# Kernel optimization log

Measured on AMD Instinct MI355X. Metric: run time of the kernel, lower is better.

## Reference

```python
import jax, jax.numpy as jnp
import numpy as np

N = 50000      # nodes
E = 800000     # edges (before self-loops)
F_IN = 512     # input features
H = 8          # heads (layer 1)
C = 32         # hidden per head
CLS = 40       # classes


def setup_inputs() -> dict:
    key = jax.random.key(0)
    ks = jax.random.split(key, 10)
    small = lambda k, shape: jax.random.normal(k, shape, jnp.float32) * 0.05
    return {
        "x": jax.random.normal(ks[0], (N, F_IN), jnp.float32),
        "edge_index": jax.random.randint(ks[1], (2, E), 0, N, jnp.int32),
        # layer 1 params (GATConv: F_IN -> C per head, 8 heads, concat)
        "W1": small(ks[2], (F_IN, H * C)),
        "a_src1": small(ks[3], (H, C)),
        "a_dst1": small(ks[4], (H, C)),
        "b1": jnp.zeros((H * C,), jnp.float32),
        # layer 2 params (GATConv: H*C -> CLS, 1 head)
        "W2": small(ks[5], (H * C, CLS)),
        "a_src2": small(ks[6], (1, CLS)),
        "a_dst2": small(ks[7], (1, CLS)),
        "b2": jnp.zeros((CLS,), jnp.float32),
    }


def gat_conv(x, W, a_src, a_dst, b, src, dst, n):
    """PyG-style GATConv (negative_slope=0.2); self-loops already in src/dst."""
    h_, c_ = a_src.shape
    h = (x @ W).reshape(n, h_, c_)                       # [N, H, C]
    alpha_src = jnp.einsum('nhc,hc->nh', h, a_src)       # [N, H]
    alpha_dst = jnp.einsum('nhc,hc->nh', h, a_dst)       # [N, H]
    e = jax.nn.leaky_relu(alpha_src[src] + alpha_dst[dst], 0.2)  # [E', H]
    # segment softmax over incoming edges of each destination node
    m = jax.lax.stop_gradient(jax.ops.segment_max(e, dst, num_segments=n))
    ex = jnp.exp(e - m[dst])
    den = jax.ops.segment_sum(ex, dst, num_segments=n)
    alpha = ex / (den[dst] + 1e-16)                      # [E', H]
    out = jax.ops.segment_sum(h[src] * alpha[:, :, None], dst, num_segments=n)
    return out.reshape(n, h_ * c_) + b


def reference(x, edge_index, W1, a_src1, a_dst1, b1, W2, a_src2, a_dst2, b2):
    n = x.shape[0]
    loop = jnp.arange(n, dtype=edge_index.dtype)
    src = jnp.concatenate([edge_index[0], loop])  # add self-loops (PyG default)
    dst = jnp.concatenate([edge_index[1], loop])
    # dropout is identity at inference
    h = jax.nn.elu(gat_conv(x, W1, a_src1, a_dst1, b1, src, dst, n))
    out = gat_conv(h, W2, a_src2, a_dst2, b2, src, dst, n)
    return jax.nn.log_softmax(out, axis=1)
```

## Files before the change

kernel.cpp:

```cpp
#include <hip/hip_runtime.h>
#include <hip/hip_bf16.h>
#include <math.h>

constexpr int NN  = 50000;
constexpr int NE  = 800000;
constexpr int EP  = NE + NN;
constexpr int FIN = 512;
constexpr int NH  = 8;
constexpr int NC  = 32;
constexpr int HC  = NH * NC;
constexpr int CLS = 40;
constexpr int CLSP = 48;
constexpr int NGB = (NN + 63) / 64;
constexpr int NSCB = (EP + 255) / 256;
constexpr int CVTW_ITEMS = HC * (FIN / 8) + CLSP * HC;
constexpr int CVTW_B = (CVTW_ITEMS + 255) / 256;

typedef __attribute__((ext_vector_type(8))) __bf16 bf16x8;
typedef __attribute__((ext_vector_type(4))) __bf16 bf16x4;
typedef __attribute__((ext_vector_type(4))) float f32x4;
typedef __attribute__((ext_vector_type(2))) float f32x2;

__device__ inline bf16x8 cvt8v(const f32x4 a, const f32x4 b) {
  bf16x8 o;
  o[0] = (__bf16)a.x; o[1] = (__bf16)a.y; o[2] = (__bf16)a.z; o[3] = (__bf16)a.w;
  o[4] = (__bf16)b.x; o[5] = (__bf16)b.y; o[6] = (__bf16)b.z; o[7] = (__bf16)b.w;
  return o;
}

__device__ inline unsigned char to_fp8(float f) {
  int pk = __builtin_amdgcn_cvt_pk_fp8_f32(f, f, 0, false);
  return (unsigned char)(pk & 0xff);
}

__device__ inline float from_fp8(unsigned char b) {
  f32x2 v = __builtin_amdgcn_cvt_pk_f32_fp8((unsigned)b, false);
  return v.x;
}

__global__ void k_prep(const int* __restrict__ ei, int* __restrict__ deg,
                       const float* __restrict__ W1, const float* __restrict__ W2,
                       __bf16* __restrict__ Wt, __bf16* __restrict__ W2t) {
  if (blockIdx.x < NSCB) {
    int e = blockIdx.x * 256 + threadIdx.x;
    if (e >= EP) return;
    int d = (e < NE) ? ei[NE + e] : (e - NE);
    atomicAdd(&deg[d], 1);
    return;
  }
  int t = (blockIdx.x - NSCB) * 256 + threadIdx.x;
  if (t < HC * (FIN / 8)) {
    int c = t >> 6, kq = (t & 63) * 8;
    bf16x8 o;
#pragma unroll
    for (int j = 0; j < 8; ++j) o[j] = (__bf16)W1[(size_t)(kq + j) * HC + c];
    *(bf16x8*)&Wt[(size_t)c * FIN + kq] = o;
  } else if (t < CVTW_ITEMS) {
    int u = t - HC * (FIN / 8);
    int c = u >> 8, k = u & 255;
    W2t[u] = (c < CLS) ? (__bf16)W2[(size_t)k * CLS + c] : (__bf16)0.f;
  }
}

__global__ __launch_bounds__(1024) void k_scan1(const int* __restrict__ deg,
                                                int* __restrict__ rowptr1,
                                                int* __restrict__ bsum, int n) {
  __shared__ int sm[1024];
  int i = blockIdx.x * 1024 + threadIdx.x;
  int v = (i < n) ? deg[i] : 0;
  sm[threadIdx.x] = v;
  __syncthreads();
  for (int off = 1; off < 1024; off <<= 1) {
    int t = (threadIdx.x >= off) ? sm[threadIdx.x - off] : 0;
    __syncthreads();
    sm[threadIdx.x] += t;
    __syncthreads();
  }
  if (i < n) rowptr1[i] = sm[threadIdx.x];
  if (threadIdx.x == 1023) bsum[blockIdx.x] = sm[1023];
}

__global__ void k_scan2(int* __restrict__ bsum, int nb) {
  int lane = threadIdx.x;
  int v = (lane < nb) ? bsum[lane] : 0;
#pragma unroll
  for (int off = 1; off < 64; off <<= 1) {
    int t = __shfl_up(v, off);
    if (lane >= off) v += t;
  }
  int ex = __shfl_up(v, 1);
  if (lane == 0) ex = 0;
  if (lane < nb) bsum[lane] = ex;
}

__global__ void k_scan3(int* __restrict__ rowptr, const int* __restrict__ bsum,
                        int* __restrict__ cursor, int n) {
  int i = blockIdx.x * 256 + threadIdx.x;
  if (i == 0) { rowptr[0] = 0; cursor[0] = 0; }
  if (i < n) {
    int v = rowptr[i + 1] + bsum[i >> 10];
    rowptr[i + 1] = v;
    if (i + 1 < n) cursor[i + 1] = v;
  }
}

__global__ __launch_bounds__(256) void k_gemm1_scatter(
    const float* __restrict__ X, const __bf16* __restrict__ Wt,
    const float* __restrict__ a_s1, const float* __restrict__ a_d1,
    unsigned char* __restrict__ Hout, float* __restrict__ asrc1,
    float* __restrict__ adst1,
    const int* __restrict__ ei, int* __restrict__ cursor,
    unsigned short* __restrict__ srcS) {
  __shared__ __align__(16) float Xp[2][4096];
  const int tid = threadIdx.x;

  if (blockIdx.x >= NGB) {
    int e = (blockIdx.x - NGB) * 256 + tid;
    if (e < EP) {
      int s, d;
      if (e < NE) { s = ei[e]; d = ei[NE + e]; } else { s = d = e - NE; }
      int p = atomicAdd(&cursor[d], 1);
      srcS[p] = (unsigned short)s;
    }
    return;
  }

  const int lane = tid & 63;
  const int w    = tid >> 6;
  const int wn   = w * 64;
  const int bm   = blockIdx.x * 64;
  const int l15  = lane & 15, lg = lane >> 4;

  const int srow_l  = (lane >> 4);
  const int sslot   = (l15 >> 1);
  const int shalf   = (lane & 1);

  f32x4 acc[4][4] = {};

  auto issue = [&](int c, int buf) {
#pragma unroll
    for (int jj = 0; jj < 4; ++jj) {
      const int j = w * 4 + jj;
      const int row_l = 4 * j + srow_l;
      const int rowG = min(bm + row_l, NN - 1);
      const int g = sslot ^ (row_l & 7);
      const float* src = X + (size_t)rowG * FIN + c * 64 + g * 8 + shalf * 4;
      __builtin_amdgcn_global_load_lds(
          (const __attribute__((address_space(1))) void*)src,
          (__attribute__((address_space(3))) void*)(&Xp[buf][j * 256]), 16, 0, 0);
    }
  };

  issue(0, 0);
  for (int c = 0; c < 8; ++c) {
    const int cur = c & 1;
    __syncthreads();
    if (c < 7) issue(c + 1, cur ^ 1);

#pragma unroll
    for (int kh = 0; kh < 2; ++kh) {
      const int kb = lg + 4 * kh;
      bf16x8 bv[4];
#pragma unroll
      for (int ni = 0; ni < 4; ++ni)
        bv[ni] = *(const bf16x8*)(Wt + (size_t)(wn + ni * 16 + l15) * FIN
                                     + c * 64 + kb * 8);
#pragma unroll
      for (int mi = 0; mi < 4; ++mi) {
        int r = mi * 16 + l15;
        int fo = r * 64 + ((kb ^ (r & 7)) << 3);
        f32x4 alo = *(const f32x4*)&Xp[cur][fo];
        f32x4 ahi = *(const f32x4*)&Xp[cur][fo + 4];
        bf16x8 av = cvt8v(alo, ahi);
#pragma unroll
        for (int ni = 0; ni < 4; ++ni)
          acc[mi][ni] = __builtin_amdgcn_mfma_f32_16x16x32_bf16(
              av, bv[ni], acc[mi][ni], 0, 0, 0);
      }
    }
    __syncthreads();
  }

  const int hbase = 2 * w;
#pragma unroll
  for (int hh = 0; hh < 2; ++hh) {
    float asA = a_s1[(hbase + hh) * NC + l15];
    float asB = a_s1[(hbase + hh) * NC + 16 + l15];
    float adA = a_d1[(hbase + hh) * NC + l15];
    float adB = a_d1[(hbase + hh) * NC + 16 + l15];
    float vs = 0.f, vd = 0.f;
#pragma unroll
    for (int mi = 0; mi < 4; ++mi) {
#pragma unroll
      for (int r = 0; r < 4; ++r) {
        float ps = acc[mi][2 * hh][r] * asA + acc[mi][2 * hh + 1][r] * asB;
        float pd = acc[mi][2 * hh][r] * adA + acc[mi][2 * hh + 1][r] * adB;
#pragma unroll
        for (int off = 1; off < 16; off <<= 1) {
          ps += __shfl_xor(ps, off, 64);
          pd += __shfl_xor(pd, off, 64);
        }
        if (l15 == mi * 4 + r) { vs = ps; vd = pd; }
      }
    }
    int rw = bm + (l15 >> 2) * 16 + lg * 4 + (l15 & 3);
    if (rw < NN) {
      asrc1[(size_t)rw * NH + hbase + hh] = vs;
      adst1[(size_t)rw * NH + hbase + hh] = vd;
    }
  }

#pragma unroll
  for (int mi = 0; mi < 4; ++mi) {
#pragma unroll
    for (int ni = 0; ni < 4; ++ni) {
      int col = wn + ni * 16 + l15;
#pragma unroll
      for (int r = 0; r < 4; ++r) {
        int row = bm + mi * 16 + lg * 4 + r;
        if (row < NN) Hout[(size_t)row * HC + col] = to_fp8(acc[mi][ni][r]);
      }
    }
  }
}

__global__ __launch_bounds__(256) void k_agg1(const unsigned char* __restrict__ h1f8,
                                              const float* __restrict__ asrc,
                                              const float* __restrict__ adst,
                                              const unsigned short* __restrict__ srcS,
                                              const int* __restrict__ rowptr,
                                              const float* __restrict__ b1,
                                              __bf16* __restrict__ helu) {
  int wave = (blockIdx.x * 256 + threadIdx.x) >> 6;
  int lane = threadIdx.x & 63;
  if (wave >= NN) return;
  int lo = rowptr[wave], hi = rowptr[wave + 1];
  int head = lane >> 3;
  int hw   = lane & 7;
  float adstv = adst[wave * NH + head];
  float ad2   = adst[wave * NH + hw];
  float4 acc = {0.f, 0.f, 0.f, 0.f};
  float den = 0.f;

  for (int base = lo; base < hi; base += 64) {
    int cnt = hi - base; if (cnt > 64) cnt = 64;
    int sv = (lane < cnt) ? (int)srcS[base + lane] : 0;
    int j = 0;
    for (; j + 8 <= cnt; j += 8) {
      int se = __shfl(sv, j + head);
      float v = asrc[se * NH + hw] + ad2;
      v = v > 0.f ? v : 0.2f * v;
      float wv = __expf(v);
      int s[8]; unsigned int hv[8];
#pragma unroll
      for (int u = 0; u < 8; ++u) s[u] = __shfl(sv, j + u);
#pragma unroll
      for (int u = 0; u < 8; ++u)
        hv[u] = *(const unsigned int*)&h1f8[(size_t)s[u] * HC + lane * 4];
#pragma unroll
      for (int u = 0; u < 8; ++u) {
        float wu = __shfl(wv, u * 8 + head);
        f32x2 lo2 = __builtin_amdgcn_cvt_pk_f32_fp8(hv[u], false);
        f32x2 hi2 = __builtin_amdgcn_cvt_pk_f32_fp8(hv[u], true);
        acc.x += wu * lo2.x;
        acc.y += wu * lo2.y;
        acc.z += wu * hi2.x;
        acc.w += wu * hi2.y;
        den += wu;
      }
    }
    for (; j < cnt; ++j) {
      int s = __shfl(sv, j);
      float v = asrc[s * NH + head] + adstv;
      v = v > 0.f ? v : 0.2f * v;
      float w = __expf(v);
      unsigned int hv = *(const unsigned int*)&h1f8[(size_t)s * HC + lane * 4];
      f32x2 lo2 = __builtin_amdgcn_cvt_pk_f32_fp8(hv, false);
      f32x2 hi2 = __builtin_amdgcn_cvt_pk_f32_fp8(hv, true);
      acc.x += w * lo2.x;
      acc.y += w * lo2.y;
      acc.z += w * hi2.x;
      acc.w += w * hi2.y;
      den += w;
    }
  }

  float inv = 1.f / (den + 1e-16f);
  float4 bb = *(const float4*)&b1[lane * 4];
  float o[4] = {acc.x * inv + bb.x, acc.y * inv + bb.y,
                acc.z * inv + bb.z, acc.w * inv + bb.w};
  bf16x4 ov;
#pragma unroll
  for (int j2 = 0; j2 < 4; ++j2) {
    float e = o[j2] > 0.f ? o[j2] : expm1f(o[j2]);
    ov[j2] = (__bf16)e;
  }
  *(bf16x4*)&helu[(size_t)wave * HC + lane * 4] = ov;
}

__global__ __launch_bounds__(256) void k_gemm2m(const __bf16* __restrict__ A,
                                                const __bf16* __restrict__ W2t,
                                                const float* __restrict__ a_s2,
                                                const float* __restrict__ a_d2,
                                                unsigned char* __restrict__ h2p,
                                                float* __restrict__ asrc2,
                                                float* __restrict__ adst2) {
  __shared__ __align__(16) __bf16 As[128 * 8 * 8];
  __shared__ __align__(16) __bf16 Bsh[CLSP * 33 * 8];
  const int tid  = threadIdx.x;
  const int lane = tid & 63;
  const int w    = tid >> 6;
  const int wm   = w * 32;
  const int bm   = blockIdx.x * 128;

  const int l3 = lane >> 3;
  const int l7 = lane & 7;
  const int kb_src = l7 ^ l3;

  for (int s = tid; s < CLSP * 32; s += 256) {
    int c = s >> 5, kb = s & 31;
    *(bf16x8*)(Bsh + (size_t)(c * 33 + kb) * 8) =
        *(const bf16x8*)(W2t + (size_t)c * HC + kb * 8);
  }

  f32x4 acc[2][3] = {};

  for (int step = 0; step < 4; ++step) {
    const int k0 = step * 64;
#pragma unroll
    for (int q = 0; q < 4; ++q) {
      const int inst = w * 4 + q;
      const int r = inst * 8 + l3;
      const int arow = min(bm + r, NN - 1);
      const __bf16* ga = A + (size_t)arow * HC + k0 + kb_src * 8;
      __builtin_amdgcn_global_load_lds(
          (const __attribute__((address_space(1))) void*)ga,
          (__attribute__((address_space(3))) void*)(As + inst * 512), 16, 0, 0);
    }
    __syncthreads();

    const int l15 = lane & 15, lg = lane >> 4;
#pragma unroll
    for (int kh = 0; kh < 2; ++kh) {
      const int kbl = lg + 4 * kh;
      const int kbg = step * 8 + kbl;
      bf16x8 av[2], bv[3];
#pragma unroll
      for (int mi = 0; mi < 2; ++mi) {
        int r = wm + mi * 16 + l15;
        av[mi] = *(const bf16x8*)(As + (size_t)(r * 8 + (kbl ^ (r & 7))) * 8);
      }
#pragma unroll
      for (int ni = 0; ni < 3; ++ni) {
        int c = ni * 16 + l15;
        bv[ni] = *(const bf16x8*)(Bsh + (size_t)(c * 33 + kbg) * 8);
      }
#pragma unroll
      for (int mi = 0; mi < 2; ++mi)
#pragma unroll
        for (int ni = 0; ni < 3; ++ni)
          acc[mi][ni] = __builtin_amdgcn_mfma_f32_16x16x32_bf16(
              av[mi], bv[ni], acc[mi][ni], 0, 0, 0);
    }
    __syncthreads();
  }

  const int l15 = lane & 15, lg = lane >> 4;

  {
    int c0 = l15, c1 = 16 + l15, c2 = 32 + l15;
    float as0 = a_s2[c0], as1 = a_s2[c1], as2v = (c2 < CLS) ? a_s2[c2] : 0.f;
    float ad0 = a_d2[c0], ad1 = a_d2[c1], ad2v = (c2 < CLS) ? a_d2[c2] : 0.f;
    float vs = 0.f, vd = 0.f;
#pragma unroll
    for (int mi = 0; mi < 2; ++mi) {
#pragma unroll
      for (int r = 0; r < 4; ++r) {
        float ps = acc[mi][0][r] * as0 + acc[mi][1][r] * as1 + acc[mi][2][r] * as2v;
        float pd = acc[mi][0][r] * ad0 + acc[mi][1][r] * ad1 + acc[mi][2][r] * ad2v;
#pragma unroll
        for (int off = 1; off < 16; off <<= 1) {
          ps += __shfl_xor(ps, off, 64);
          pd += __shfl_xor(pd, off, 64);
        }
        if (l15 == mi * 4 + r) { vs = ps; vd = pd; }
      }
    }
    int rw = bm + wm + (l15 >> 2) * 16 + lg * 4 + (l15 & 3);
    if (l15 < 8 && rw < NN) {
      asrc2[rw] = vs;
      adst2[rw] = vd;
    }
  }

#pragma unroll
  for (int mi = 0; mi < 2; ++mi) {
#pragma unroll
    for (int ni = 0; ni < 3; ++ni) {
      int col = ni * 16 + l15;
      if (col >= CLS) continue;
#pragma unroll
      for (int r = 0; r < 4; ++r) {
        int row = bm + wm + mi * 16 + lg * 4 + r;
        if (row < NN) h2p[(size_t)row * 64 + col] = to_fp8(acc[mi][ni][r]);
      }
    }
  }
}

__global__ __launch_bounds__(256) void k_agg2(const unsigned char* __restrict__ h2p,
                                              const float* __restrict__ asrc,
                                              const float* __restrict__ adst,
                                              const unsigned short* __restrict__ srcS,
                                              const int* __restrict__ rowptr,
                                              const float* __restrict__ b2,
                                              float* __restrict__ out) {
  int wave = (blockIdx.x * 256 + threadIdx.x) >> 6;
  int lane = threadIdx.x & 63;
  if (wave >= NN) return;
  int lo = rowptr[wave], hi = rowptr[wave + 1];
  bool act = lane < CLS;
  float adstv = adst[wave];
  float acc = 0.f, den = 0.f;

  for (int base = lo; base < hi; base += 64) {
    int cnt = hi - base; if (cnt > 64) cnt = 64;
    int sv = (lane < cnt) ? (int)srcS[base + lane] : 0;
    float v = asrc[sv] + adstv;
    v = v > 0.f ? v : 0.2f * v;
    float wv = __expf(v);
    int j = 0;
    for (; j + 8 <= cnt; j += 8) {
      int s[8]; float hval[8];
#pragma unroll
      for (int u = 0; u < 8; ++u) s[u] = __shfl(sv, j + u);
#pragma unroll
      for (int u = 0; u < 8; ++u)
        hval[u] = act ? from_fp8(h2p[(size_t)s[u] * 64 + lane]) : 0.f;
#pragma unroll
      for (int u = 0; u < 8; ++u) {
        float wu = __shfl(wv, j + u);
        acc += wu * hval[u];
        den += wu;
      }
    }
    for (; j < cnt; ++j) {
      int s = __shfl(sv, j);
      float wu = __shfl(wv, j);
      if (act) acc += wu * from_fp8(h2p[(size_t)s * 64 + lane]);
      den += wu;
    }
  }

  float o = act ? (acc / (den + 1e-16f) + b2[lane]) : -INFINITY;
  float m = o;
#pragma unroll
  for (int off = 32; off; off >>= 1) m = fmaxf(m, __shfl_xor(m, off, 64));
  float ex = act ? __expf(o - m) : 0.f;
  float ssum = ex;
#pragma unroll
  for (int off = 32; off; off >>= 1) ssum += __shfl_xor(ssum, off, 64);
  if (act) out[(size_t)wave * CLS + lane] = o - m - logf(ssum);
}

extern "C" void kernel_launch(void* const* d_in, const int* in_sizes, int n_in,
                              void* d_out, int out_size, void* d_ws, size_t ws_size,
                              hipStream_t stream) {
  const float* x      = (const float*)d_in[0];
  const int*   ei     = (const int*)d_in[1];
  const float* W1     = (const float*)d_in[2];
  const float* a_src1 = (const float*)d_in[3];
  const float* a_dst1 = (const float*)d_in[4];
  const float* b1     = (const float*)d_in[5];
  const float* W2     = (const float*)d_in[6];
  const float* a_src2 = (const float*)d_in[7];
  const float* a_dst2 = (const float*)d_in[8];
  const float* b2     = (const float*)d_in[9];
  float* out = (float*)d_out;

  char* p = (char*)d_ws;
  auto alloc = [&](size_t bytes) {
    char* r = p;
    p += (bytes + 255) & ~size_t(255);
    return r;
  };
  unsigned char* h1f8 = (unsigned char*)alloc((size_t)NN * HC);
  __bf16* helu  = (__bf16*)alloc((size_t)NN * HC * 2);
  __bf16* Wt    = (__bf16*)alloc((size_t)HC * FIN * 2);
  __bf16* W2t   = (__bf16*)alloc((size_t)CLSP * HC * 2);
  unsigned char* h2p = (unsigned char*)alloc((size_t)NN * 64);
  float*  asrc1 = (float*)alloc((size_t)NN * NH * 4);
  float*  adst1 = (float*)alloc((size_t)NN * NH * 4);
  float*  asrc2 = (float*)alloc((size_t)NN * 4);
  float*  adst2 = (float*)alloc((size_t)NN * 4);
  unsigned short* srcS = (unsigned short*)alloc((size_t)EP * 2);
  int*    deg   = (int*)alloc((size_t)NN * 4);
  int*    cursor= (int*)alloc((size_t)NN * 4);
  int*    rowptr= (int*)alloc((size_t)(NN + 1) * 4);
  int*    bsum  = (int*)alloc(256 * 4);

  hipMemsetAsync(deg, 0, (size_t)NN * 4, stream);

  const int nbScan = (NN + 1023) / 1024;
  k_prep<<<NSCB + CVTW_B, 256, 0, stream>>>(ei, deg, W1, W2, Wt, W2t);
  k_scan1<<<nbScan, 1024, 0, stream>>>(deg, rowptr + 1, bsum, NN);
  k_scan2<<<1, 64, 0, stream>>>(bsum, nbScan);
  k_scan3<<<(NN + 255) / 256, 256, 0, stream>>>(rowptr, bsum, cursor, NN);

  k_gemm1_scatter<<<NGB + NSCB, 256, 0, stream>>>(x, Wt, a_src1, a_dst1,
                                                  h1f8, asrc1, adst1,
                                                  ei, cursor, srcS);

  k_agg1<<<(NN + 3) / 4, 256, 0, stream>>>(h1f8, asrc1, adst1, srcS, rowptr, b1, helu);

  k_gemm2m<<<(NN + 127) / 128, 256, 0, stream>>>(helu, W2t, a_src2, a_dst2,
                                                 h2p, asrc2, adst2);

  k_agg2<<<(NN + 3) / 4, 256, 0, stream>>>(h2p, asrc2, adst2, srcS, rowptr, b2, out);
}
```

Before: 226.3 us.

## Restructure CSR build: histogram with per-edge rank overlapped with GEMM1, then atomic-free scatter

The degree histogram moves into the GEMM1 kernel and records each edge's atomic rank. After the scan, a separate pass places sources at rowptr[d]+rank[e] with no atomics. This removes the second atomic pass and the memset, and overlaps the histogram atomics with the GEMM. The cost is an extra launch and a 3.4 MB rank buffer written and read back.

```diff
diff --git a/kernel.cpp b/kernel.cpp
--- a/kernel.cpp
+++ b/kernel.cpp
@@ -11,8 +11,9 @@
 constexpr int HC  = NH * NC;
 constexpr int CLS = 40;
 constexpr int CLSP = 48;
-constexpr int NGB = (NN + 63) / 64;
+constexpr int NGB  = (NN + 63) / 64;
 constexpr int NSCB = (EP + 255) / 256;
+constexpr int DEGB = (NN + 255) / 256;
 constexpr int CVTW_ITEMS = HC * (FIN / 8) + CLSP * HC;
 constexpr int CVTW_B = (CVTW_ITEMS + 255) / 256;
 
@@ -38,17 +39,15 @@
   return v.x;
 }
 
-__global__ void k_prep(const int* __restrict__ ei, int* __restrict__ deg,
+__global__ void k_pre0(int* __restrict__ deg,
                        const float* __restrict__ W1, const float* __restrict__ W2,
                        __bf16* __restrict__ Wt, __bf16* __restrict__ W2t) {
-  if (blockIdx.x < NSCB) {
-    int e = blockIdx.x * 256 + threadIdx.x;
-    if (e >= EP) return;
-    int d = (e < NE) ? ei[NE + e] : (e - NE);
-    atomicAdd(&deg[d], 1);
+  if (blockIdx.x < DEGB) {
+    int i = blockIdx.x * 256 + threadIdx.x;
+    if (i < NN) deg[i] = 0;
     return;
   }
-  int t = (blockIdx.x - NSCB) * 256 + threadIdx.x;
+  int t = (blockIdx.x - DEGB) * 256 + threadIdx.x;
   if (t < HC * (FIN / 8)) {
     int c = t >> 6, kq = (t & 63) * 8;
     bf16x8 o;
@@ -59,6 +58,124 @@
     int u = t - HC * (FIN / 8);
     int c = u >> 8, k = u & 255;
     W2t[u] = (c < CLS) ? (__bf16)W2[(size_t)k * CLS + c] : (__bf16)0.f;
+  }
+}
+
+__global__ __launch_bounds__(256) void k_gemm1_hist(
+    const float* __restrict__ X, const __bf16* __restrict__ Wt,
+    const float* __restrict__ a_s1, const float* __restrict__ a_d1,
+    unsigned char* __restrict__ Hout, float* __restrict__ asrc1,
+    float* __restrict__ adst1,
+    const int* __restrict__ ei, int* __restrict__ deg,
+    int* __restrict__ rank) {
+  __shared__ __align__(16) float Xp[2][4096];
+  const int tid = threadIdx.x;
+
+  if (blockIdx.x >= NGB) {
+    int e = (blockIdx.x - NGB) * 256 + tid;
+    if (e < EP) {
+      int d = (e < NE) ? ei[NE + e] : (e - NE);
+      rank[e] = atomicAdd(&deg[d], 1);
+    }
+    return;
+  }
+
+  const int lane = tid & 63;
+  const int w    = tid >> 6;
+  const int wn   = w * 64;
+  const int bm   = blockIdx.x * 64;
+  const int l15  = lane & 15, lg = lane >> 4;
+
+  const int srow_l  = (lane >> 4);
+  const int sslot   = (l15 >> 1);
+  const int shalf   = (lane & 1);
+
+  f32x4 acc[4][4] = {};
+
+  auto issue = [&](int c, int buf) {
+#pragma unroll
+    for (int jj = 0; jj < 4; ++jj) {
+      const int j = w * 4 + jj;
+      const int row_l = 4 * j + srow_l;
+      const int rowG = min(bm + row_l, NN - 1);
+      const int g = sslot ^ (row_l & 7);
+      const float* src = X + (size_t)rowG * FIN + c * 64 + g * 8 + shalf * 4;
+      __builtin_amdgcn_global_load_lds(
+          (const __attribute__((address_space(1))) void*)src,
+          (__attribute__((address_space(3))) void*)(&Xp[buf][j * 256]), 16, 0, 0);
+    }
+  };
+
+  issue(0, 0);
+  for (int c = 0; c < 8; ++c) {
+    const int cur = c & 1;
+    __syncthreads();
+    if (c < 7) issue(c + 1, cur ^ 1);
+
+#pragma unroll
+    for (int kh = 0; kh < 2; ++kh) {
+      const int kb = lg + 4 * kh;
+      bf16x8 bv[4];
+#pragma unroll
+      for (int ni = 0; ni < 4; ++ni)
+        bv[ni] = *(const bf16x8*)(Wt + (size_t)(wn + ni * 16 + l15) * FIN
+                                     + c * 64 + kb * 8);
+#pragma unroll
+      for (int mi = 0; mi < 4; ++mi) {
+        int r = mi * 16 + l15;
+        int fo = r * 64 + ((kb ^ (r & 7)) << 3);
+        f32x4 alo = *(const f32x4*)&Xp[cur][fo];
+        f32x4 ahi = *(const f32x4*)&Xp[cur][fo + 4];
+        bf16x8 av = cvt8v(alo, ahi);
+#pragma unroll
+        for (int ni = 0; ni < 4; ++ni)
+          acc[mi][ni] = __builtin_amdgcn_mfma_f32_16x16x32_bf16(
+              av, bv[ni], acc[mi][ni], 0, 0, 0);
+      }
+    }
+    __syncthreads();
+  }
+
+  const int hbase = 2 * w;
+#pragma unroll
+  for (int hh = 0; hh < 2; ++hh) {
+    float asA = a_s1[(hbase + hh) * NC + l15];
+    float asB = a_s1[(hbase + hh) * NC + 16 + l15];
+    float adA = a_d1[(hbase + hh) * NC + l15];
+    float adB = a_d1[(hbase + hh) * NC + 16 + l15];
+    float vs = 0.f, vd = 0.f;
+#pragma unroll
+    for (int mi = 0; mi < 4; ++mi) {
+#pragma unroll
+      for (int r = 0; r < 4; ++r) {
+        float ps = acc[mi][2 * hh][r] * asA + acc[mi][2 * hh + 1][r] * asB;
+        float pd = acc[mi][2 * hh][r] * adA + acc[mi][2 * hh + 1][r] * adB;
+#pragma unroll
+        for (int off = 1; off < 16; off <<= 1) {
+          ps += __shfl_xor(ps, off, 64);
+          pd += __shfl_xor(pd, off, 64);
+        }
+        if (l15 == mi * 4 + r) { vs = ps; vd = pd; }
+      }
+    }
+    int rw = bm + (l15 >> 2) * 16 + lg * 4 + (l15 & 3);
+    if (rw < NN) {
+      asrc1[(size_t)rw * NH + hbase + hh] = vs;
+      adst1[(size_t)rw * NH + hbase + hh] = vd;
+    }
+  }
+
+#pragma unroll
+  for (int mi = 0; mi < 4; ++mi) {
+#pragma unroll
+    for (int ni = 0; ni < 4; ++ni) {
+      int col = wn + ni * 16 + l15;
+#pragma unroll
+      for (int r = 0; r < 4; ++r) {
+        int row = bm + mi * 16 + lg * 4 + r;
+        if (row < NN) Hout[(size_t)row * HC + col] = to_fp8(acc[mi][ni][r]);
+      }
+    }
   }
 }
 
@@ -93,135 +210,20 @@
   if (lane < nb) bsum[lane] = ex;
 }
 
-__global__ void k_scan3(int* __restrict__ rowptr, const int* __restrict__ bsum,
-                        int* __restrict__ cursor, int n) {
+__global__ void k_scan3(int* __restrict__ rowptr, const int* __restrict__ bsum, int n) {
   int i = blockIdx.x * 256 + threadIdx.x;
-  if (i == 0) { rowptr[0] = 0; cursor[0] = 0; }
-  if (i < n) {
-    int v = rowptr[i + 1] + bsum[i >> 10];
-    rowptr[i + 1] = v;
-    if (i + 1 < n) cursor[i + 1] = v;
-  }
-}
-
-__global__ __launch_bounds__(256) void k_gemm1_scatter(
-    const float* __restrict__ X, const __bf16* __restrict__ Wt,
-    const float* __restrict__ a_s1, const float* __restrict__ a_d1,
-    unsigned char* __restrict__ Hout, float* __restrict__ asrc1,
-    float* __restrict__ adst1,
-    const int* __restrict__ ei, int* __restrict__ cursor,
-    unsigned short* __restrict__ srcS) {
-  __shared__ __align__(16) float Xp[2][4096];
-  const int tid = threadIdx.x;
-
-  if (blockIdx.x >= NGB) {
-    int e = (blockIdx.x - NGB) * 256 + tid;
-    if (e < EP) {
-      int s, d;
-      if (e < NE) { s = ei[e]; d = ei[NE + e]; } else { s = d = e - NE; }
-      int p = atomicAdd(&cursor[d], 1);
-      srcS[p] = (unsigned short)s;
-    }
-    return;
-  }
-
-  const int lane = tid & 63;
-  const int w    = tid >> 6;
-  const int wn   = w * 64;
-  const int bm   = blockIdx.x * 64;
-  const int l15  = lane & 15, lg = lane >> 4;
-
-  const int srow_l  = (lane >> 4);
-  const int sslot   = (l15 >> 1);
-  const int shalf   = (lane & 1);
-
-  f32x4 acc[4][4] = {};
-
-  auto issue = [&](int c, int buf) {
-#pragma unroll
-    for (int jj = 0; jj < 4; ++jj) {
-      const int j = w * 4 + jj;
-      const int row_l = 4 * j + srow_l;
-      const int rowG = min(bm + row_l, NN - 1);
-      const int g = sslot ^ (row_l & 7);
-      const float* src = X + (size_t)rowG * FIN + c * 64 + g * 8 + shalf * 4;
-      __builtin_amdgcn_global_load_lds(
-          (const __attribute__((address_space(1))) void*)src,
-          (__attribute__((address_space(3))) void*)(&Xp[buf][j * 256]), 16, 0, 0);
-    }
-  };
-
-  issue(0, 0);
-  for (int c = 0; c < 8; ++c) {
-    const int cur = c & 1;
-    __syncthreads();
-    if (c < 7) issue(c + 1, cur ^ 1);
-
-#pragma unroll
-    for (int kh = 0; kh < 2; ++kh) {
-      const int kb = lg + 4 * kh;
-      bf16x8 bv[4];
-#pragma unroll
-      for (int ni = 0; ni < 4; ++ni)
-        bv[ni] = *(const bf16x8*)(Wt + (size_t)(wn + ni * 16 + l15) * FIN
-                                     + c * 64 + kb * 8);
-#pragma unroll
-      for (int mi = 0; mi < 4; ++mi) {
-        int r = mi * 16 + l15;
-        int fo = r * 64 + ((kb ^ (r & 7)) << 3);
-        f32x4 alo = *(const f32x4*)&Xp[cur][fo];
-        f32x4 ahi = *(const f32x4*)&Xp[cur][fo + 4];
-        bf16x8 av = cvt8v(alo, ahi);
-#pragma unroll
-        for (int ni = 0; ni < 4; ++ni)
-          acc[mi][ni] = __builtin_amdgcn_mfma_f32_16x16x32_bf16(
-              av, bv[ni], acc[mi][ni], 0, 0, 0);
-      }
-    }
-    __syncthreads();
-  }
-
-  const int hbase = 2 * w;
-#pragma unroll
-  for (int hh = 0; hh < 2; ++hh) {
-    float asA = a_s1[(hbase + hh) * NC + l15];
-    float asB = a_s1[(hbase + hh) * NC + 16 + l15];
-    float adA = a_d1[(hbase + hh) * NC + l15];
-    float adB = a_d1[(hbase + hh) * NC + 16 + l15];
-    float vs = 0.f, vd = 0.f;
-#pragma unroll
-    for (int mi = 0; mi < 4; ++mi) {
-#pragma unroll
-      for (int r = 0; r < 4; ++r) {
-        float ps = acc[mi][2 * hh][r] * asA + acc[mi][2 * hh + 1][r] * asB;
-        float pd = acc[mi][2 * hh][r] * adA + acc[mi][2 * hh + 1][r] * adB;
-#pragma unroll
-        for (int off = 1; off < 16; off <<= 1) {
-          ps += __shfl_xor(ps, off, 64);
-          pd += __shfl_xor(pd, off, 64);
-        }
-        if (l15 == mi * 4 + r) { vs = ps; vd = pd; }
-      }
-    }
-    int rw = bm + (l15 >> 2) * 16 + lg * 4 + (l15 & 3);
-    if (rw < NN) {
-      asrc1[(size_t)rw * NH + hbase + hh] = vs;
-      adst1[(size_t)rw * NH + hbase + hh] = vd;
-    }
-  }
-
-#pragma unroll
-  for (int mi = 0; mi < 4; ++mi) {
-#pragma unroll
-    for (int ni = 0; ni < 4; ++ni) {
-      int col = wn + ni * 16 + l15;
-#pragma unroll
-      for (int r = 0; r < 4; ++r) {
-        int row = bm + mi * 16 + lg * 4 + r;
-        if (row < NN) Hout[(size_t)row * HC + col] = to_fp8(acc[mi][ni][r]);
-      }
-    }
-  }
+  if (i == 0) rowptr[0] = 0;
+  if (i < n) rowptr[i + 1] += bsum[i >> 10];
+}
+
+__global__ void k_pass2(const int* __restrict__ ei, const int* __restrict__ rank,
+                        const int* __restrict__ rowptr,
+                        unsigned short* __restrict__ srcS) {
+  int e = blockIdx.x * 256 + threadIdx.x;
+  if (e >= EP) return;
+  int s, d;
+  if (e < NE) { s = ei[e]; d = ei[NE + e]; } else { s = d = e - NE; }
+  srcS[rowptr[d] + rank[e]] = (unsigned short)s;
 }
 
 __global__ __launch_bounds__(256) void k_agg1(const unsigned char* __restrict__ h1f8,
@@ -494,22 +496,24 @@
   float*  asrc2 = (float*)alloc((size_t)NN * 4);
   float*  adst2 = (float*)alloc((size_t)NN * 4);
   unsigned short* srcS = (unsigned short*)alloc((size_t)EP * 2);
+  int*    rank  = (int*)alloc((size_t)EP * 4);
   int*    deg   = (int*)alloc((size_t)NN * 4);
-  int*    cursor= (int*)alloc((size_t)NN * 4);
   int*    rowptr= (int*)alloc((size_t)(NN + 1) * 4);
   int*    bsum  = (int*)alloc(256 * 4);
 
-  hipMemsetAsync(deg, 0, (size_t)NN * 4, stream);
-
   const int nbScan = (NN + 1023) / 1024;
-  k_prep<<<NSCB + CVTW_B, 256, 0, stream>>>(ei, deg, W1, W2, Wt, W2t);
+
+  k_pre0<<<DEGB + CVTW_B, 256, 0, stream>>>(deg, W1, W2, Wt, W2t);
+
+  k_gemm1_hist<<<NGB + NSCB, 256, 0, stream>>>(x, Wt, a_src1, a_dst1,
+                                               h1f8, asrc1, adst1,
+                                               ei, deg, rank);
+
   k_scan1<<<nbScan, 1024, 0, stream>>>(deg, rowptr + 1, bsum, NN);
   k_scan2<<<1, 64, 0, stream>>>(bsum, nbScan);
-  k_scan3<<<(NN + 255) / 256, 256, 0, stream>>>(rowptr, bsum, cursor, NN);
-
-  k_gemm1_scatter<<<NGB + NSCB, 256, 0, stream>>>(x, Wt, a_src1, a_dst1,
-                                                  h1f8, asrc1, adst1,
-                                                  ei, cursor, srcS);
+  k_scan3<<<(NN + 255) / 256, 256, 0, stream>>>(rowptr, bsum, NN);
+
+  k_pass2<<<NSCB, 256, 0, stream>>>(ei, rank, rowptr, srcS);
 
   k_agg1<<<(NN + 3) / 4, 256, 0, stream>>>(h1f8, asrc1, adst1, srcS, rowptr, b1, helu);
 
```

Result: faster. 193.6 us (-14.5%).
